# Performance work log

Hardware: AMD Instinct MI355X
Metric: run time of the kernel (lower is better)

The kernel has to match this reference:

```python
import jax, jax.numpy as jnp
import numpy as np

N_NODES = 50000
N_EDGES = 600000
F_DIM = 128


def setup_inputs() -> dict:
    key = jax.random.key(0)
    k_x, k_e, k_w1, k_b1, k_w2, k_b2 = jax.random.split(key, 6)
    x = jax.random.normal(k_x, (N_NODES, F_DIM), dtype=jnp.float32)
    edge_index = jax.random.randint(k_e, (2, N_EDGES), 0, N_NODES, dtype=jnp.int64)
    # nn.Linear-style params (weight is [out, in])
    s1 = 1.0 / np.sqrt(F_DIM)
    w1 = jax.random.uniform(k_w1, (128, F_DIM), jnp.float32, -s1, s1)
    b1 = jax.random.uniform(k_b1, (128,), jnp.float32, -s1, s1)
    s2 = 1.0 / np.sqrt(128)
    w2 = jax.random.uniform(k_w2, (F_DIM, 128), jnp.float32, -s2, s2)
    b2 = jax.random.uniform(k_b2, (F_DIM,), jnp.float32, -s2, s2)
    return {"x": x, "edge_index": edge_index, "w1": w1, "b1": b1, "w2": w2, "b2": b2}


def reference(x, edge_index, w1, b1, w2, b2):
    n = x.shape[0]
    # add_self_loops: append (i, i) for every node
    loops = jnp.arange(n, dtype=edge_index.dtype)
    src = jnp.concatenate([edge_index[0], loops])  # [E + N]
    dst = jnp.concatenate([edge_index[1], loops])  # [E + N]

    def conv(h):
        h = h @ w1.T + b1          # [N, 128]
        h = h @ w2.T + b2          # [N, F]
        msgs = h[src]              # gather source features [E+N, F]
        return jax.ops.segment_sum(msgs, dst, num_segments=n)  # scatter-add

    h = conv(conv(x))
    return jax.nn.log_softmax(h, axis=1)
```

## Files before the change

### kernel.cpp

```cpp
#include <hip/hip_runtime.h>
#include <hip/hip_bf16.h>

#define N_NODES 50000
#define N_EDGES 600000
#define F 128

#define GEMM_BLOCKS 782
#define NBINS 196
#define NHB 128
#define EPB 4688

typedef unsigned short bf16_t;
typedef __attribute__((ext_vector_type(8))) short short8v;
typedef __attribute__((ext_vector_type(8))) unsigned short ushort8v;
typedef __attribute__((ext_vector_type(4))) float f32x4;

__device__ inline float bf2f(bf16_t u) {
    union { unsigned int i; float f; } c;
    c.i = ((unsigned int)u) << 16;
    return c.f;
}
__device__ inline bf16_t f2bf(float f) {
    union { float f; unsigned int i; } c;
    c.f = f;
    unsigned int lsb = (c.i >> 16) & 1;
    c.i += 0x7fffu + lsb;
    return (bf16_t)(c.i >> 16);
}

__global__ void k_fuse(const float* __restrict__ w1, const float* __restrict__ b1,
                       const float* __restrict__ w2, const float* __restrict__ b2,
                       float* __restrict__ Wc, float* __restrict__ bc) {
    int p = blockIdx.x;
    int j = threadIdx.x;
    float s = 0.f;
    for (int o = 0; o < F; ++o) s = fmaf(w2[p * F + o], w1[o * F + j], s);
    Wc[p * F + j] = s;
    if (j == 0) {
        float t = b2[p];
        for (int o = 0; o < F; ++o) t = fmaf(w2[p * F + o], b1[o], t);
        bc[p] = t;
    }
}

__global__ __launch_bounds__(256)
void k_fuse2h(const float* __restrict__ Wc, const float* __restrict__ bc,
              bf16_t* __restrict__ Mbf, float* __restrict__ v1,
              const int* __restrict__ dst, int* __restrict__ cnt2) {
    int bid = blockIdx.x;
    int tid = threadIdx.x;
    if (bid < 128) {
        if (tid < 128) {
            int k = bid, p = tid;
            float s = 0.f;
            for (int o = 0; o < F; ++o) s = fmaf(Wc[p * F + o], Wc[o * F + k], s);
            Mbf[p * F + k] = f2bf(s);
            if (k == 0) {
                float t = 0.f;
                for (int o = 0; o < F; ++o) t = fmaf(Wc[p * F + o], bc[o], t);
                v1[p] = t;
            }
        }
        return;
    }
    __shared__ int hist[NBINS];
    int hb = bid - 128;
    for (int b = tid; b < NBINS; b += 256) hist[b] = 0;
    __syncthreads();
    int e0 = hb * EPB;
    int e1 = min(e0 + EPB, N_EDGES);
    for (int e = e0 + tid; e < e1; e += 256) atomicAdd(&hist[dst[e] >> 8], 1);
    __syncthreads();
    for (int b = tid; b < NBINS; b += 256) cnt2[b * NHB + hb] = hist[b];
}

__global__ __launch_bounds__(1024)
void k_binscan(const int* __restrict__ cnt2, int* __restrict__ wofs2,
               int* __restrict__ binofs) {
    __shared__ int wtot[16];
    const int NV = NBINS * NHB;
    const int CH = 25;
    int t = threadIdx.x;
    int lane = t & 63, wv = t >> 6;
    int base = t * CH;
    int s = 0;
    for (int i = 0; i < CH; ++i) {
        int idx = base + i;
        if (idx < NV) s += cnt2[idx];
    }
    int incl = s;
#pragma unroll
    for (int o = 1; o < 64; o <<= 1) {
        int u = __shfl_up(incl, o);
        if (lane >= o) incl += u;
    }
    if (lane == 63) wtot[wv] = incl;
    __syncthreads();
    if (t == 0) {
        int r = 0;
        for (int w = 0; w < 16; ++w) { int x = wtot[w]; wtot[w] = r; r += x; }
    }
    __syncthreads();
    int run = incl - s + wtot[wv];
    for (int i = 0; i < CH; ++i) {
        int idx = base + i;
        if (idx < NV) {
            int w = cnt2[idx];
            wofs2[idx] = run;
            if ((idx & (NHB - 1)) == 0) binofs[idx >> 7] = run;
            run += w;
        }
    }
    if (t == 0) binofs[NBINS] = N_EDGES;
}

__global__ __launch_bounds__(256, 4)
void k_mainB(const float* __restrict__ X, const bf16_t* __restrict__ Mbf,
             bf16_t* __restrict__ G,
             const int* __restrict__ src, const int* __restrict__ dst,
             const int* __restrict__ wofs2, unsigned int* __restrict__ ebuf) {
    const int bid = blockIdx.x;
    const int tid = threadIdx.x;

    if (bid >= GEMM_BLOCKS) {
        __shared__ int cur[NBINS];
        int hb = bid - GEMM_BLOCKS;
        for (int b = tid; b < NBINS; b += 256) cur[b] = wofs2[b * NHB + hb];
        __syncthreads();
        int e0 = hb * EPB;
        int e1 = min(e0 + EPB, N_EDGES);
        for (int e = e0 + tid; e < e1; e += 256) {
            int d = dst[e];
            int s = src[e];
            int b = d >> 8;
            int pos = atomicAdd(&cur[b], 1);
            ebuf[pos] = ((unsigned int)(d & 255) << 16) | (unsigned int)s;
        }
        return;
    }

    __shared__ unsigned short Xs[64 * 128];
    const int row0 = bid * 64;

    for (int idx = tid; idx < 1024; idx += 256) {
        int r = idx >> 4, c = idx & 15;
        int grow = row0 + r;
        float4 va = {0.f, 0.f, 0.f, 0.f}, vb = {0.f, 0.f, 0.f, 0.f};
        if (grow < N_NODES) {
            const float4* xr = (const float4*)(X + (size_t)grow * F);
            va = xr[2 * c];
            vb = xr[2 * c + 1];
        }
        ushort8v u;
        u[0] = f2bf(va.x); u[1] = f2bf(va.y); u[2] = f2bf(va.z); u[3] = f2bf(va.w);
        u[4] = f2bf(vb.x); u[5] = f2bf(vb.y); u[6] = f2bf(vb.z); u[7] = f2bf(vb.w);
        *(ushort8v*)&Xs[r * 128 + (((c ^ (r & 7)) << 3))] = u;
    }
    __syncthreads();

    const int wid = tid >> 6;
    const int lane = tid & 63;
    const int wr = wid >> 1;
    const int wc = wid & 1;
    const int l15 = lane & 15;
    const int l4 = lane >> 4;
    const int sw = (l15 & 7);

    f32x4 acc[2][4] = {};

#pragma unroll
    for (int kc = 0; kc < 4; ++kc) {
        const int cS = ((kc * 4 + l4) ^ sw) << 3;
        short8v a0 = *(const short8v*)&Xs[(wr * 32 + 0 * 16 + l15) * 128 + cS];
        short8v a1 = *(const short8v*)&Xs[(wr * 32 + 1 * 16 + l15) * 128 + cS];
        const bf16_t* mb = Mbf + (size_t)(wc * 64 + l15) * F + kc * 32 + 8 * l4;
        short8v b0 = *(const short8v*)(mb + 0 * 16 * F);
        short8v b1 = *(const short8v*)(mb + 1 * 16 * F);
        short8v b2 = *(const short8v*)(mb + 2 * 16 * F);
        short8v b3 = *(const short8v*)(mb + 3 * 16 * F);
        acc[0][0] = __builtin_amdgcn_mfma_f32_16x16x32_bf16(a0, b0, acc[0][0], 0, 0, 0);
        acc[0][1] = __builtin_amdgcn_mfma_f32_16x16x32_bf16(a0, b1, acc[0][1], 0, 0, 0);
        acc[0][2] = __builtin_amdgcn_mfma_f32_16x16x32_bf16(a0, b2, acc[0][2], 0, 0, 0);
        acc[0][3] = __builtin_amdgcn_mfma_f32_16x16x32_bf16(a0, b3, acc[0][3], 0, 0, 0);
        acc[1][0] = __builtin_amdgcn_mfma_f32_16x16x32_bf16(a1, b0, acc[1][0], 0, 0, 0);
        acc[1][1] = __builtin_amdgcn_mfma_f32_16x16x32_bf16(a1, b1, acc[1][1], 0, 0, 0);
        acc[1][2] = __builtin_amdgcn_mfma_f32_16x16x32_bf16(a1, b2, acc[1][2], 0, 0, 0);
        acc[1][3] = __builtin_amdgcn_mfma_f32_16x16x32_bf16(a1, b3, acc[1][3], 0, 0, 0);
    }

#pragma unroll
    for (int mt = 0; mt < 2; ++mt) {
#pragma unroll
        for (int nt = 0; nt < 4; ++nt) {
#pragma unroll
            for (int r = 0; r < 4; ++r) {
                int grow = row0 + wr * 32 + mt * 16 + l4 * 4 + r;
                if (grow < N_NODES) {
                    int gcol = wc * 64 + nt * 16 + l15;
                    G[(size_t)grow * F + gcol] = f2bf(acc[mt][nt][r]);
                }
            }
        }
    }
}

__global__ __launch_bounds__(256)
void k_fine(const unsigned int* __restrict__ ebuf, const int* __restrict__ binofs,
            int* __restrict__ cnt, int* __restrict__ rofs,
            unsigned short* __restrict__ csr) {
    __shared__ int hcnt[256];
    __shared__ int cur2[256];
    __shared__ int wtot[4];
    int b = blockIdx.x, t = threadIdx.x;
    int r0 = binofs[b];
    int m = binofs[b + 1] - r0;

    hcnt[t] = 0;
    __syncthreads();
    for (int i = t; i < m; i += 256) atomicAdd(&hcnt[ebuf[r0 + i] >> 16], 1);
    __syncthreads();

    int v = hcnt[t];
    int lane = t & 63, wv = t >> 6;
    int incl = v;
#pragma unroll
    for (int o = 1; o < 64; o <<= 1) {
        int u = __shfl_up(incl, o);
        if (lane >= o) incl += u;
    }
    if (lane == 63) wtot[wv] = incl;
    __syncthreads();
    if (t == 0) {
        int r = 0;
        for (int w = 0; w < 4; ++w) { int x = wtot[w]; wtot[w] = r; r += x; }
    }
    __syncthreads();
    int excl = incl - v + wtot[wv];

    int node = b * 256 + t;
    if (node < N_NODES) { cnt[node] = v; rofs[node] = r0 + excl; }
    if (node == N_NODES) rofs[N_NODES] = N_EDGES;
    cur2[t] = excl;
    __syncthreads();

    for (int i = t; i < m; i += 256) {
        unsigned int u = ebuf[r0 + i];
        int d8 = u >> 16;
        int s = u & 0xFFFF;
        int slot = atomicAdd(&cur2[d8], 1);
        csr[r0 + slot] = (unsigned short)s;
    }
}

__global__ __launch_bounds__(256)
void k_agg(const bf16_t* __restrict__ H, const int* __restrict__ rofs,
           const unsigned short* __restrict__ csr, bf16_t* __restrict__ O,
           int n_rows) {
    int tid = threadIdx.x;
    int lane = tid & 15;
    int node = blockIdx.x * 16 + (tid >> 4);
    if (node >= n_rows) return;

    int r0 = rofs[node];
    int deg = rofs[node + 1] - r0;

    ushort8v u = ((const ushort8v*)(H + (size_t)node * F))[lane];
    float a0 = bf2f(u[0]), a1 = bf2f(u[1]), a2 = bf2f(u[2]), a3 = bf2f(u[3]);
    float a4 = bf2f(u[4]), a5 = bf2f(u[5]), a6 = bf2f(u[6]), a7 = bf2f(u[7]);

    const unsigned short* bk = csr + r0;
    int i = 0;
    for (; i + 4 <= deg; i += 4) {
        int s0 = bk[i + 0], s1 = bk[i + 1], s2 = bk[i + 2], s3 = bk[i + 3];
        ushort8v u0 = ((const ushort8v*)(H + (size_t)s0 * F))[lane];
        ushort8v u1 = ((const ushort8v*)(H + (size_t)s1 * F))[lane];
        ushort8v u2 = ((const ushort8v*)(H + (size_t)s2 * F))[lane];
        ushort8v u3 = ((const ushort8v*)(H + (size_t)s3 * F))[lane];
        a0 += bf2f(u0[0]) + bf2f(u1[0]) + bf2f(u2[0]) + bf2f(u3[0]);
        a1 += bf2f(u0[1]) + bf2f(u1[1]) + bf2f(u2[1]) + bf2f(u3[1]);
        a2 += bf2f(u0[2]) + bf2f(u1[2]) + bf2f(u2[2]) + bf2f(u3[2]);
        a3 += bf2f(u0[3]) + bf2f(u1[3]) + bf2f(u2[3]) + bf2f(u3[3]);
        a4 += bf2f(u0[4]) + bf2f(u1[4]) + bf2f(u2[4]) + bf2f(u3[4]);
        a5 += bf2f(u0[5]) + bf2f(u1[5]) + bf2f(u2[5]) + bf2f(u3[5]);
        a6 += bf2f(u0[6]) + bf2f(u1[6]) + bf2f(u2[6]) + bf2f(u3[6]);
        a7 += bf2f(u0[7]) + bf2f(u1[7]) + bf2f(u2[7]) + bf2f(u3[7]);
    }
    for (; i < deg; ++i) {
        ushort8v uv = ((const ushort8v*)(H + (size_t)bk[i] * F))[lane];
        a0 += bf2f(uv[0]); a1 += bf2f(uv[1]); a2 += bf2f(uv[2]); a3 += bf2f(uv[3]);
        a4 += bf2f(uv[4]); a5 += bf2f(uv[5]); a6 += bf2f(uv[6]); a7 += bf2f(uv[7]);
    }
    ushort8v o;
    o[0] = f2bf(a0); o[1] = f2bf(a1); o[2] = f2bf(a2); o[3] = f2bf(a3);
    o[4] = f2bf(a4); o[5] = f2bf(a5); o[6] = f2bf(a6); o[7] = f2bf(a7);
    ((ushort8v*)(O + (size_t)node * F))[lane] = o;
}

__global__ __launch_bounds__(256)
void k_agg_ep(const bf16_t* __restrict__ H, const int* __restrict__ rofs,
              const unsigned short* __restrict__ csr, const int* __restrict__ cnt,
              const float* __restrict__ v1, const float* __restrict__ bc,
              float* __restrict__ O, int n_rows) {
    int tid = threadIdx.x;
    int lane = tid & 15;
    int node = blockIdx.x * 16 + (tid >> 4);
    if (node >= n_rows) return;

    int r0 = rofs[node];
    int deg = rofs[node + 1] - r0;

    ushort8v u = ((const ushort8v*)(H + (size_t)node * F))[lane];
    float a0 = bf2f(u[0]), a1 = bf2f(u[1]), a2 = bf2f(u[2]), a3 = bf2f(u[3]);
    float a4 = bf2f(u[4]), a5 = bf2f(u[5]), a6 = bf2f(u[6]), a7 = bf2f(u[7]);

    const unsigned short* bk = csr + r0;

    int sdi = (lane == 0) ? (deg + 1) : 0;
    for (int j = lane; j < deg; j += 16) sdi += cnt[bk[j]] + 1;

    int i = 0;
    for (; i + 4 <= deg; i += 4) {
        int s0 = bk[i + 0], s1 = bk[i + 1], s2 = bk[i + 2], s3 = bk[i + 3];
        ushort8v u0 = ((const ushort8v*)(H + (size_t)s0 * F))[lane];
        ushort8v u1 = ((const ushort8v*)(H + (size_t)s1 * F))[lane];
        ushort8v u2 = ((const ushort8v*)(H + (size_t)s2 * F))[lane];
        ushort8v u3 = ((const ushort8v*)(H + (size_t)s3 * F))[lane];
        a0 += bf2f(u0[0]) + bf2f(u1[0]) + bf2f(u2[0]) + bf2f(u3[0]);
        a1 += bf2f(u0[1]) + bf2f(u1[1]) + bf2f(u2[1]) + bf2f(u3[1]);
        a2 += bf2f(u0[2]) + bf2f(u1[2]) + bf2f(u2[2]) + bf2f(u3[2]);
        a3 += bf2f(u0[3]) + bf2f(u1[3]) + bf2f(u2[3]) + bf2f(u3[3]);
        a4 += bf2f(u0[4]) + bf2f(u1[4]) + bf2f(u2[4]) + bf2f(u3[4]);
        a5 += bf2f(u0[5]) + bf2f(u1[5]) + bf2f(u2[5]) + bf2f(u3[5]);
        a6 += bf2f(u0[6]) + bf2f(u1[6]) + bf2f(u2[6]) + bf2f(u3[6]);
        a7 += bf2f(u0[7]) + bf2f(u1[7]) + bf2f(u2[7]) + bf2f(u3[7]);
    }
    for (; i < deg; ++i) {
        ushort8v uv = ((const ushort8v*)(H + (size_t)bk[i] * F))[lane];
        a0 += bf2f(uv[0]); a1 += bf2f(uv[1]); a2 += bf2f(uv[2]); a3 += bf2f(uv[3]);
        a4 += bf2f(uv[4]); a5 += bf2f(uv[5]); a6 += bf2f(uv[6]); a7 += bf2f(uv[7]);
    }

#pragma unroll
    for (int o = 8; o; o >>= 1) sdi += __shfl_xor(sdi, o);
    float sdn = (float)sdi;
    float dn = (float)(deg + 1);
    float4 v1a = ((const float4*)v1)[2 * lane], v1b = ((const float4*)v1)[2 * lane + 1];
    float4 bca = ((const float4*)bc)[2 * lane], bcb = ((const float4*)bc)[2 * lane + 1];
    a0 += sdn * v1a.x + dn * bca.x;
    a1 += sdn * v1a.y + dn * bca.y;
    a2 += sdn * v1a.z + dn * bca.z;
    a3 += sdn * v1a.w + dn * bca.w;
    a4 += sdn * v1b.x + dn * bcb.x;
    a5 += sdn * v1b.y + dn * bcb.y;
    a6 += sdn * v1b.z + dn * bcb.z;
    a7 += sdn * v1b.w + dn * bcb.w;

    float m = fmaxf(fmaxf(fmaxf(a0, a1), fmaxf(a2, a3)),
                    fmaxf(fmaxf(a4, a5), fmaxf(a6, a7)));
#pragma unroll
    for (int o = 8; o; o >>= 1) m = fmaxf(m, __shfl_xor(m, o));
    float s = expf(a0 - m) + expf(a1 - m) + expf(a2 - m) + expf(a3 - m)
            + expf(a4 - m) + expf(a5 - m) + expf(a6 - m) + expf(a7 - m);
#pragma unroll
    for (int o = 8; o; o >>= 1) s += __shfl_xor(s, o);
    float lse = m + logf(s);
    float4 oa, ob;
    oa.x = a0 - lse; oa.y = a1 - lse; oa.z = a2 - lse; oa.w = a3 - lse;
    ob.x = a4 - lse; ob.y = a5 - lse; ob.z = a6 - lse; ob.w = a7 - lse;
    ((float4*)(O + (size_t)node * F))[2 * lane] = oa;
    ((float4*)(O + (size_t)node * F))[2 * lane + 1] = ob;
}

extern "C" void kernel_launch(void* const* d_in, const int* in_sizes, int n_in,
                              void* d_out, int out_size, void* d_ws, size_t ws_size,
                              hipStream_t stream) {
    const float* x  = (const float*)d_in[0];
    const int* ei   = (const int*)d_in[1];
    const float* w1 = (const float*)d_in[2];
    const float* b1 = (const float*)d_in[3];
    const float* w2 = (const float*)d_in[4];
    const float* b2 = (const float*)d_in[5];
    float* out = (float*)d_out;

    const int* src = ei;
    const int* dst = ei + N_EDGES;

    float* ws        = (float*)d_ws;
    float* Wc        = ws;
    float* bc        = ws + 16384;
    float* v1        = ws + 16512;
    bf16_t* Mbf      = (bf16_t*)(ws + 16640);
    int*   cnt       = (int*)(ws + 24832);
    int*   rofs      = (int*)(ws + 74880);
    int*   cnt2      = (int*)(ws + 124928);
    int*   wofs2     = (int*)(ws + 150016);
    int*   binofs    = (int*)(ws + 175104);
    unsigned int* ebuf = (unsigned int*)(ws + 175360);
    unsigned short* csr = (unsigned short*)(ws + 775360);
    bf16_t* g        = (bf16_t*)(ws + 1075360);
    bf16_t* a1       = (bf16_t*)(ws + 4275360);

    const int node_grid = (N_NODES + 15) / 16;

    k_fuse<<<128, 128, 0, stream>>>(w1, b1, w2, b2, Wc, bc);
    k_fuse2h<<<128 + NHB, 256, 0, stream>>>(Wc, bc, Mbf, v1, dst, cnt2);
    k_binscan<<<1, 1024, 0, stream>>>(cnt2, wofs2, binofs);
    k_mainB<<<GEMM_BLOCKS + NHB, 256, 0, stream>>>(x, Mbf, g, src, dst,
                                                   wofs2, ebuf);
    k_fine<<<NBINS, 256, 0, stream>>>(ebuf, binofs, cnt, rofs, csr);
    k_agg<<<node_grid, 256, 0, stream>>>(g, rofs, csr, a1, N_NODES);
    k_agg_ep<<<node_grid, 256, 0, stream>>>(a1, rofs, csr, cnt, v1, bc, out, N_NODES);
}
```

Measured before the change: 134.5 us.

## Stage edge partition in LDS and write bin runs contiguously

Edge-partition blocks in k_mainB now do a local bin scan, scatter packed (dst,src) pairs into shared memory sorted by coarse bin, and then copy each bin run to its global slot in ebuf. Before, every edge was scattered straight to global memory. The number of partition blocks is halved and edges per block doubled, and the packed word now carries the full destination, so k_fine masks the low 8 bits. The cost is a much larger static shared-memory allocation, which also applies to the GEMM blocks of the same kernel and may limit occupancy.

```diff
diff --git a/kernel.cpp b/kernel.cpp
--- a/kernel.cpp
+++ b/kernel.cpp
@@ -7,8 +7,8 @@
 
 #define GEMM_BLOCKS 782
 #define NBINS 196
-#define NHB 128
-#define EPB 4688
+#define NHB 64
+#define EPB 9375
 
 typedef unsigned short bf16_t;
 typedef __attribute__((ext_vector_type(8))) short short8v;
@@ -79,7 +79,7 @@
                int* __restrict__ binofs) {
     __shared__ int wtot[16];
     const int NV = NBINS * NHB;
-    const int CH = 25;
+    const int CH = 13;
     int t = threadIdx.x;
     int lane = t & 63, wv = t >> 6;
     int base = t * CH;
@@ -107,7 +107,7 @@
         if (idx < NV) {
             int w = cnt2[idx];
             wofs2[idx] = run;
-            if ((idx & (NHB - 1)) == 0) binofs[idx >> 7] = run;
+            if ((idx & (NHB - 1)) == 0) binofs[idx / NHB] = run;
             run += w;
         }
     }
@@ -118,28 +118,65 @@
 void k_mainB(const float* __restrict__ X, const bf16_t* __restrict__ Mbf,
              bf16_t* __restrict__ G,
              const int* __restrict__ src, const int* __restrict__ dst,
-             const int* __restrict__ wofs2, unsigned int* __restrict__ ebuf) {
+             const int* __restrict__ cnt2, const int* __restrict__ wofs2,
+             unsigned int* __restrict__ ebuf) {
+    __shared__ __align__(16) unsigned char smem[EPB * 4 + 3 * NBINS * 4 + 16];
     const int bid = blockIdx.x;
     const int tid = threadIdx.x;
 
     if (bid >= GEMM_BLOCKS) {
-        __shared__ int cur[NBINS];
+        unsigned int* pairs = (unsigned int*)smem;
+        int* cur  = (int*)(smem + EPB * 4);
+        int* lofs = cur + NBINS;
+        int* gofs = lofs + NBINS;
+        int* wt4  = gofs + NBINS;
         int hb = bid - GEMM_BLOCKS;
-        for (int b = tid; b < NBINS; b += 256) cur[b] = wofs2[b * NHB + hb];
+
+        int c = 0;
+        if (tid < NBINS) {
+            c = cnt2[tid * NHB + hb];
+            gofs[tid] = wofs2[tid * NHB + hb];
+        }
+        int lane = tid & 63, wv = tid >> 6;
+        int incl = c;
+#pragma unroll
+        for (int o = 1; o < 64; o <<= 1) {
+            int u = __shfl_up(incl, o);
+            if (lane >= o) incl += u;
+        }
+        if (lane == 63) wt4[wv] = incl;
         __syncthreads();
+        if (tid == 0) {
+            int r = 0;
+            for (int w = 0; w < 4; ++w) { int x = wt4[w]; wt4[w] = r; r += x; }
+        }
+        __syncthreads();
+        if (tid < NBINS) {
+            int e = incl - c + wt4[wv];
+            lofs[tid] = e;
+            cur[tid] = e;
+        }
+        __syncthreads();
+
         int e0 = hb * EPB;
-        int e1 = min(e0 + EPB, N_EDGES);
-        for (int e = e0 + tid; e < e1; e += 256) {
+        for (int e = e0 + tid; e < e0 + EPB; e += 256) {
             int d = dst[e];
             int s = src[e];
-            int b = d >> 8;
-            int pos = atomicAdd(&cur[b], 1);
-            ebuf[pos] = ((unsigned int)(d & 255) << 16) | (unsigned int)s;
+            unsigned int p = ((unsigned int)d << 16) | (unsigned int)s;
+            int slot = atomicAdd(&cur[d >> 8], 1);
+            pairs[slot] = p;
+        }
+        __syncthreads();
+
+        for (int i = tid; i < EPB; i += 256) {
+            unsigned int p = pairs[i];
+            int b = p >> 24;
+            ebuf[gofs[b] + (i - lofs[b])] = p;
         }
         return;
     }
 
-    __shared__ unsigned short Xs[64 * 128];
+    unsigned short* Xs = (unsigned short*)smem;
     const int row0 = bid * 64;
 
     for (int idx = tid; idx < 1024; idx += 256) {
@@ -217,7 +254,7 @@
 
     hcnt[t] = 0;
     __syncthreads();
-    for (int i = t; i < m; i += 256) atomicAdd(&hcnt[ebuf[r0 + i] >> 16], 1);
+    for (int i = t; i < m; i += 256) atomicAdd(&hcnt[(ebuf[r0 + i] >> 16) & 255], 1);
     __syncthreads();
 
     int v = hcnt[t];
@@ -245,7 +282,7 @@
 
     for (int i = t; i < m; i += 256) {
         unsigned int u = ebuf[r0 + i];
-        int d8 = u >> 16;
+        int d8 = (u >> 16) & 255;
         int s = u & 0xFFFF;
         int slot = atomicAdd(&cur2[d8], 1);
         csr[r0 + slot] = (unsigned short)s;
@@ -393,12 +430,12 @@
     int*   cnt       = (int*)(ws + 24832);
     int*   rofs      = (int*)(ws + 74880);
     int*   cnt2      = (int*)(ws + 124928);
-    int*   wofs2     = (int*)(ws + 150016);
-    int*   binofs    = (int*)(ws + 175104);
-    unsigned int* ebuf = (unsigned int*)(ws + 175360);
-    unsigned short* csr = (unsigned short*)(ws + 775360);
-    bf16_t* g        = (bf16_t*)(ws + 1075360);
-    bf16_t* a1       = (bf16_t*)(ws + 4275360);
+    int*   wofs2     = (int*)(ws + 137728);
+    int*   binofs    = (int*)(ws + 150528);
+    unsigned int* ebuf = (unsigned int*)(ws + 150784);
+    unsigned short* csr = (unsigned short*)(ws + 750784);
+    bf16_t* g        = (bf16_t*)(ws + 1050784);
+    bf16_t* a1       = (bf16_t*)(ws + 4250784);
 
     const int node_grid = (N_NODES + 15) / 16;
 
@@ -406,7 +443,7 @@
     k_fuse2h<<<128 + NHB, 256, 0, stream>>>(Wc, bc, Mbf, v1, dst, cnt2);
     k_binscan<<<1, 1024, 0, stream>>>(cnt2, wofs2, binofs);
     k_mainB<<<GEMM_BLOCKS + NHB, 256, 0, stream>>>(x, Mbf, g, src, dst,
-                                                   wofs2, ebuf);
+                                                   cnt2, wofs2, ebuf);
     k_fine<<<NBINS, 256, 0, stream>>>(ebuf, binofs, cnt, rofs, csr);
     k_agg<<<node_grid, 256, 0, stream>>>(g, rofs, csr, a1, N_NODES);
     k_agg_ep<<<node_grid, 256, 0, stream>>>(a1, rofs, csr, cnt, v1, bc, out, N_NODES);
```

After: 121.5 us. 1.11x faster.
